# Kernel tuning notes

Hardware: AMD Instinct MI355X
Metric: run time of the kernel (lower is better)

## Reference

```python
import jax, jax.numpy as jnp
import numpy as np

H, D, Kd, Vd = 16, 1024, 64, 64
N, Mlen = 4096, 4096


def setup_inputs() -> dict:
    key = jax.random.key(0)
    ks = jax.random.split(key, 7)
    X = jax.random.normal(ks[0], (N, D), dtype=jnp.float32)
    M = jax.random.normal(ks[1], (Mlen, D), dtype=jnp.float32)
    mask = jax.random.randint(ks[2], (N, Mlen), 0, 2, dtype=jnp.int32)
    Wq = jax.random.normal(ks[3], (H, D, Kd), dtype=jnp.float32)
    Wk = jax.random.normal(ks[4], (H, D, Kd), dtype=jnp.float32)
    Wv = jax.random.normal(ks[5], (H, D, Vd), dtype=jnp.float32)
    Wo = jax.random.normal(ks[6], (H, Vd, D), dtype=jnp.float32)
    return {"X": X, "M": M, "mask": mask, "Wq": Wq, "Wk": Wk, "Wv": Wv, "Wo": Wo}


def reference(X, M, mask, Wq, Wk, Wv, Wo):
    # Projections: [h,n,k], [h,m,k], [h,m,v]
    Q = jnp.einsum('nd,hdk->hnk', X, Wq)
    K = jnp.einsum('md,hdk->hmk', M, Wk)
    V = jnp.einsum('md,hdv->hmv', M, Wv)
    # Masked attention (no scaling, matching the source)
    logits = jnp.einsum('hnk,hmk->hnm', Q, K)
    logits = jnp.where(mask[None, :, :] == 0, -jnp.inf, logits)
    weights = jax.nn.softmax(logits, axis=-1)
    O = jnp.einsum('hnm,hmv->hnv', weights, V)
    Y = jnp.einsum('hnv,hvd->nd', O, Wo)
    return Y
```

## Files before the change

kernel.cpp:

```cpp
#include <hip/hip_runtime.h>

typedef _Float16 half8 __attribute__((ext_vector_type(8)));
typedef _Float16 half4 __attribute__((ext_vector_type(4)));
typedef __fp16 fp16x2 __attribute__((ext_vector_type(2)));
typedef short short8 __attribute__((ext_vector_type(8)));
typedef short short4v __attribute__((ext_vector_type(4)));
typedef float floatx4 __attribute__((ext_vector_type(4)));

#define LOG2E 1.4426950408889634f

#define GLDS16(g, l) __builtin_amdgcn_global_load_lds( \
    (const __attribute__((address_space(1))) unsigned int*)(g), \
    (__attribute__((address_space(3))) unsigned int*)(l), 16, 0, 0)

static __device__ __forceinline__ short f2bf(float f){
  union { float f; unsigned u; } v; v.f = f;
  unsigned r = v.u + 0x7fffu + ((v.u >> 16) & 1u);
  return (short)(r >> 16);
}
static __device__ __forceinline__ float bf2f(short s){
  union { unsigned u; float f; } v; v.u = ((unsigned)(unsigned short)s) << 16;
  return v.f;
}

__global__ __launch_bounds__(256) void kconvA(const float* __restrict__ X,
                                              const float* __restrict__ Mm,
                                              short* __restrict__ XFh, short* __restrict__ XFl,
                                              short* __restrict__ MFh, short* __restrict__ MFl){
  int b = blockIdx.x;
  int t = threadIdx.x, w = t >> 6, l = t & 63, quad = l >> 4;
  int srcsel = b >> 8, ntile = b & 255;
  const float* A = srcsel ? Mm : X;
  short* oh = srcsel ? MFh : XFh;
  short* ol = srcsel ? MFl : XFl;
  int row = ntile*16 + (l & 15);
  #pragma unroll
  for (int i = 0; i < 8; i++){
    int kt = w*8 + i;
    const float* p = A + (size_t)row*1024 + kt*32 + quad*8;
    float4 v0 = *(const float4*)p, v1 = *(const float4*)(p + 4);
    float vv[8] = {v0.x,v0.y,v0.z,v0.w,v1.x,v1.y,v1.z,v1.w};
    short8 hh, ll;
    #pragma unroll
    for (int j = 0; j < 8; j++){
      short hb = f2bf(vv[j]); hh[j] = hb; ll[j] = f2bf(vv[j] - bf2f(hb));
    }
    size_t off = ((size_t)kt*256 + ntile)*512 + l*8;
    *(short8*)&oh[off] = hh;
    *(short8*)&ol[off] = ll;
  }
}

__global__ __launch_bounds__(256) void kconvW2(const float* __restrict__ Wq,
                                               const float* __restrict__ Wk,
                                               const float* __restrict__ Wv,
                                               short* __restrict__ WFh, short* __restrict__ WFl){
  __shared__ float T[128][68];
  int bidx = blockIdx.x, g = blockIdx.y;
  int mat = bidx >> 4, h = bidx & 15;
  const float* W = (mat == 0 ? Wq : (mat == 1 ? Wk : Wv)) + (size_t)h*65536;
  int t = threadIdx.x, w = t >> 6, l = t & 63, quad = (l >> 4) & 3, fl = l & 15;
  #pragma unroll
  for (int p = 0; p < 32; p++){
    int idx = p*256 + t, row = idx >> 6, col = idx & 63;
    T[row][col] = W[(size_t)(g*128 + row)*64 + col];
  }
  __syncthreads();
  for (int ktl = 0; ktl < 4; ktl++){
    short8 hh, ll;
    #pragma unroll
    for (int j = 0; j < 8; j++){
      float v = T[ktl*32 + quad*8 + j][w*16 + fl];
      short hb = f2bf(v); hh[j] = hb; ll[j] = f2bf(v - bf2f(hb));
    }
    size_t frag = ((size_t)bidx*32 + g*4 + ktl)*4 + w;
    *(short8*)&WFh[frag*512 + l*8] = hh;
    *(short8*)&WFl[frag*512 + l*8] = ll;
  }
}

__global__ __launch_bounds__(256) void kmaskpack(const int* __restrict__ mask,
                                                 unsigned* __restrict__ bits){
  int w = blockIdx.x * 256 + threadIdx.x;
  const int4* p = (const int4*)(mask + (size_t)w * 32);
  unsigned b = 0;
  #pragma unroll
  for (int i = 0; i < 8; i++){
    int4 v = p[i];
    b |= (v.x ? 1u : 0u) << (i*4);
    b |= (v.y ? 1u : 0u) << (i*4 + 1);
    b |= (v.z ? 1u : 0u) << (i*4 + 2);
    b |= (v.w ? 1u : 0u) << (i*4 + 3);
  }
  bits[w] = b;
}

__global__ __launch_bounds__(256) void ktransw(const float* __restrict__ src,
                                               short* __restrict__ dsth,
                                               int R, int C){
  __shared__ float tile[32][33];
  int r0 = blockIdx.y*32, c0 = blockIdx.x*32;
  int t = threadIdx.x, tr = t >> 3, tc = (t & 7)*4;
  const float* s = src + (size_t)(r0 + tr)*C + c0 + tc;
  #pragma unroll
  for (int i = 0; i < 4; i++) tile[tr][tc + i] = s[i];
  __syncthreads();
  short* dh = dsth + (size_t)(c0 + tr)*R + r0 + tc;
  #pragma unroll
  for (int i = 0; i < 4; i++)
    dh[i] = f2bf(tile[tc + i][tr]);
}

__global__ __launch_bounds__(256,3) void kproj3(
    const short* __restrict__ XFh, const short* __restrict__ XFl,
    const short* __restrict__ MFh, const short* __restrict__ MFl,
    const short* __restrict__ WFh, const short* __restrict__ WFl,
    _Float16* __restrict__ QFh, _Float16* __restrict__ QFl,
    _Float16* __restrict__ KFh, _Float16* __restrict__ KFl,
    _Float16* __restrict__ VF)
{
  __shared__ short AhL[4096], AlL[4096], BhL[4096], BlL[2048];
  int cb = blockIdx.y, rb = blockIdx.x;
  const bool fused = (cb >= 16);
  int h = fused ? (cb - 16) : cb;
  const short* Ah = fused ? MFh : XFh;
  const short* Al = fused ? MFl : XFl;
  int t = threadIdx.x, w = t >> 6, l = t & 63, quad = l >> 4, ln = l & 15;
  floatx4 acc[2][8] = {};
  for (int kt = 0; kt < 32; kt++){
    __syncthreads();
    size_t abase = ((size_t)kt*256 + rb*8)*512;
    #pragma unroll
    for (int i = 0; i < 2; i++){
      int cidx = i*256 + t;
      GLDS16(Ah + abase + cidx*8, &AhL[(i*256 + w*64)*8]);
      GLDS16(Al + abase + cidx*8, &AlL[(i*256 + w*64)*8]);
    }
    size_t bb0 = (((size_t)cb*32 + kt)*4)*512;
    GLDS16(WFh + bb0 + t*8, &BhL[(w*64)*8]);
    GLDS16(WFl + bb0 + t*8, &BlL[(w*64)*8]);
    if (fused){
      size_t bb1 = (((size_t)(cb + 16)*32 + kt)*4)*512;
      GLDS16(WFh + bb1 + t*8, &BhL[(256 + w*64)*8]);
    }
    __syncthreads();
    short8 ah[2], al[2];
    #pragma unroll
    for (int mt = 0; mt < 2; mt++){
      ah[mt] = *(short8*)&AhL[(w*2 + mt)*512 + l*8];
      al[mt] = *(short8*)&AlL[(w*2 + mt)*512 + l*8];
    }
    {
      short8 bh[4], bl[4];
      #pragma unroll
      for (int nt = 0; nt < 4; nt++){
        bh[nt] = *(short8*)&BhL[nt*512 + l*8];
        bl[nt] = *(short8*)&BlL[nt*512 + l*8];
      }
      #pragma unroll
      for (int mt = 0; mt < 2; mt++)
        #pragma unroll
        for (int nt = 0; nt < 4; nt++){
          acc[mt][nt] = __builtin_amdgcn_mfma_f32_16x16x32_bf16(ah[mt], bh[nt], acc[mt][nt], 0, 0, 0);
          acc[mt][nt] = __builtin_amdgcn_mfma_f32_16x16x32_bf16(ah[mt], bl[nt], acc[mt][nt], 0, 0, 0);
          acc[mt][nt] = __builtin_amdgcn_mfma_f32_16x16x32_bf16(al[mt], bh[nt], acc[mt][nt], 0, 0, 0);
        }
    }
    if (fused){
      short8 bh[4];
      #pragma unroll
      for (int nt = 0; nt < 4; nt++)
        bh[nt] = *(short8*)&BhL[(4 + nt)*512 + l*8];
      #pragma unroll
      for (int mt = 0; mt < 2; mt++)
        #pragma unroll
        for (int nt = 0; nt < 4; nt++)
          acc[mt][4+nt] = __builtin_amdgcn_mfma_f32_16x16x32_bf16(ah[mt], bh[nt], acc[mt][4+nt], 0, 0, 0);
    }
  }
  int row0 = rb*128;
  if (!fused){
    #pragma unroll
    for (int mt = 0; mt < 2; mt++)
      #pragma unroll
      for (int nt = 0; nt < 4; nt++)
        #pragma unroll
        for (int rg = 0; rg < 4; rg++){
          int n = row0 + w*32 + mt*16 + quad*4 + rg;
          int c = nt*16 + ln;
          float v = acc[mt][nt][rg] * LOG2E;
          _Float16 hi = (_Float16)v;
          _Float16 lo = (_Float16)(v - (float)hi);
          int lane2 = (n & 15) + (((c >> 3) & 3) << 4);
          size_t off = (((size_t)h*256 + (n >> 4))*2 + (c >> 5))*512 + lane2*8 + (c & 7);
          QFh[off] = hi; QFl[off] = lo;
        }
  } else {
    #pragma unroll
    for (int mt = 0; mt < 2; mt++)
      #pragma unroll
      for (int nt = 0; nt < 4; nt++)
        #pragma unroll
        for (int rg = 0; rg < 4; rg++){
          int n = row0 + w*32 + mt*16 + quad*4 + rg;
          int c = nt*16 + ln;
          float v = acc[mt][nt][rg];
          _Float16 hi = (_Float16)v;
          _Float16 lo = (_Float16)(v - (float)hi);
          int lane2 = (n & 15) + (((c >> 3) & 3) << 4);
          size_t off = (((size_t)h*256 + (n >> 4))*2 + (c >> 5))*512 + lane2*8 + (c & 7);
          KFh[off] = hi; KFl[off] = lo;
        }
    #pragma unroll
    for (int mt = 0; mt < 2; mt++)
      #pragma unroll
      for (int ntv = 0; ntv < 4; ntv++){
        union { fp16x2 h2[2]; unsigned u2[2]; } pu;
        pu.h2[0] = __builtin_amdgcn_cvt_pkrtz(acc[mt][4+ntv][0], acc[mt][4+ntv][1]);
        pu.h2[1] = __builtin_amdgcn_cvt_pkrtz(acc[mt][4+ntv][2], acc[mt][4+ntv][3]);
        size_t base = (((size_t)h*32 + rb)*16 + ntv*4 + w)*512;
        *(uint2*)&VF[base + (quad*16 + ln)*8 + mt*4] = *(uint2*)&pu.u2[0];
      }
  }
}

__global__ __launch_bounds__(256,4) void kattn8(
    const _Float16* __restrict__ QFh, const _Float16* __restrict__ QFl,
    const _Float16* __restrict__ KFh, const _Float16* __restrict__ KFl,
    const _Float16* __restrict__ VF, const unsigned* __restrict__ bits,
    short* __restrict__ Ows)
{
  __shared__ _Float16 KBh[2][4096], KBl[2][4096], VB[4096];
  int bx = blockIdx.x, h = bx & 15, qb = bx >> 4, q0 = qb*64;
  int t = threadIdx.x, w = t >> 6, l = t & 63, quad = l >> 4, ln = l & 15;

  half8 qh[2], ql[2];
  #pragma unroll
  for (int kc = 0; kc < 2; kc++){
    size_t off = (((size_t)h*256 + qb*4 + w)*2 + kc)*512 + l*8;
    qh[kc] = *(const half8*)&QFh[off];
    ql[kc] = *(const half8*)&QFl[off];
  }

  floatx4 o[4] = {};
  float mst = -1e30f, lst = 0.f;

  const size_t hb = (size_t)h*262144;
  const int cidx0 = t, cidx1 = 256 + t;
  const int ld0 = (w*64)*8, ld1 = (256 + w*64)*8;

  {
    GLDS16(KFh + hb + cidx0*8, &KBh[0][ld0]);
    GLDS16(KFh + hb + cidx1*8, &KBh[0][ld1]);
    GLDS16(KFl + hb + cidx0*8, &KBl[0][ld0]);
    GLDS16(KFl + hb + cidx1*8, &KBl[0][ld1]);
    #pragma unroll
    for (int i = 0; i < 2; i++){
      int cidx = i*256 + t;
      int lu = cidx >> 6, uoff = (cidx & 63)*8;
      int gu = (lu >> 1)*4 + (lu & 1);
      GLDS16(VF + hb + (size_t)gu*512 + uoff, &VB[(i*256 + w*64)*8]);
    }
  }
  uint2 mwv = *(const uint2*)&bits[(size_t)(q0 + w*16 + ln)*128];
  __syncthreads();

  int cur = 0;
  for (int kt = 0; kt < 64; kt++){
    int ktn = (kt + 1) & 63;
    size_t kbn = hb + (size_t)ktn*4096;
    GLDS16(KFh + kbn + cidx0*8, &KBh[cur^1][ld0]);
    GLDS16(KFh + kbn + cidx1*8, &KBh[cur^1][ld1]);
    GLDS16(KFl + kbn + cidx0*8, &KBl[cur^1][ld0]);
    GLDS16(KFl + kbn + cidx1*8, &KBl[cur^1][ld1]);
    uint2 mwn = *(const uint2*)&bits[(size_t)(q0 + w*16 + ln)*128 + ktn*2];

    floatx4 st[4] = {};
    __builtin_amdgcn_s_setprio(1);
    #pragma unroll
    for (int kc = 0; kc < 2; kc++)
      #pragma unroll
      for (int m8 = 0; m8 < 4; m8++){
        half8 kh = *(half8*)&KBh[cur][(m8*2 + kc)*512 + l*8];
        half8 kl = *(half8*)&KBl[cur][(m8*2 + kc)*512 + l*8];
        st[m8] = __builtin_amdgcn_mfma_f32_16x16x32_f16(kh, qh[kc], st[m8], 0, 0, 0);
        st[m8] = __builtin_amdgcn_mfma_f32_16x16x32_f16(kl, qh[kc], st[m8], 0, 0, 0);
        st[m8] = __builtin_amdgcn_mfma_f32_16x16x32_f16(kh, ql[kc], st[m8], 0, 0, 0);
      }
    __builtin_amdgcn_s_setprio(0);

    {
      const unsigned mwp[2] = {mwv.x, mwv.y};
      #pragma unroll
      for (int m8 = 0; m8 < 4; m8++){
        unsigned nib = (mwp[m8 >> 1] >> ((m8 & 1)*16 + quad*4)) & 15u;
        #pragma unroll
        for (int rg = 0; rg < 4; rg++)
          if (!((nib >> rg) & 1u)) st[m8][rg] = -1e30f;
      }
      float a0 = fmaxf(fmaxf(st[0][0], st[0][1]), fmaxf(st[0][2], st[0][3]));
      float a1 = fmaxf(fmaxf(st[1][0], st[1][1]), fmaxf(st[1][2], st[1][3]));
      float a2 = fmaxf(fmaxf(st[2][0], st[2][1]), fmaxf(st[2][2], st[2][3]));
      float a3 = fmaxf(fmaxf(st[3][0], st[3][1]), fmaxf(st[3][2], st[3][3]));
      float mx = fmaxf(fmaxf(a0, a1), fmaxf(a2, a3));
      mx = fmaxf(mx, __shfl_xor(mx, 16));
      mx = fmaxf(mx, __shfl_xor(mx, 32));
      if (__any(mx > mst + 8.0f)){
        float mnew = fmaxf(mst, mx);
        float alpha = exp2f(mst - mnew);
        mst = mnew;
        lst *= alpha;
        #pragma unroll
        for (int vt = 0; vt < 4; vt++) o[vt] *= alpha;
      }
      float ssum = 0.f;
      #pragma unroll
      for (int m8 = 0; m8 < 4; m8++)
        #pragma unroll
        for (int rg = 0; rg < 4; rg++){
          float p = exp2f(st[m8][rg] - mst);
          st[m8][rg] = p; ssum += p;
        }
      lst += ssum;
    }
    mwv = mwn;

    __syncthreads();

    __builtin_amdgcn_s_setprio(1);
    #pragma unroll
    for (int p = 0; p < 2; p++){
      half8 vfp[4];
      #pragma unroll
      for (int vt = 0; vt < 4; vt++)
        vfp[vt] = *(half8*)&VB[((vt*2 + p)*512) + l*8];
      #pragma unroll
      for (int sub = 0; sub < 2; sub++){
        int m8 = p*2 + sub;
        union { fp16x2 h2[2]; half4 h4; } pu;
        pu.h2[0] = __builtin_amdgcn_cvt_pkrtz(st[m8][0], st[m8][1]);
        pu.h2[1] = __builtin_amdgcn_cvt_pkrtz(st[m8][2], st[m8][3]);
        #pragma unroll
        for (int vt = 0; vt < 4; vt++){
          half4 va = sub ? __builtin_shufflevector(vfp[vt], vfp[vt], 4,5,6,7)
                         : __builtin_shufflevector(vfp[vt], vfp[vt], 0,1,2,3);
          o[vt] = __builtin_amdgcn_mfma_f32_16x16x16f16(va, pu.h4, o[vt], 0, 0, 0);
        }
      }
    }
    __builtin_amdgcn_s_setprio(0);

    __syncthreads();

    {
      size_t vbn = hb + (size_t)(ktn >> 1)*8192;
      int vhalf = (ktn & 1)*2;
      #pragma unroll
      for (int i = 0; i < 2; i++){
        int cidx = i*256 + t;
        int lu = cidx >> 6, uoff = (cidx & 63)*8;
        int gu = (lu >> 1)*4 + vhalf + (lu & 1);
        GLDS16(VF + vbn + (size_t)gu*512 + uoff, &VB[(i*256 + w*64)*8]);
      }
    }
    cur ^= 1;
  }

  {
    lst += __shfl_xor(lst, 16);
    lst += __shfl_xor(lst, 32);
    float inv = (lst > 0.f) ? (1.f / lst) : 0.f;
    int n = q0 + w*16 + ln;
    #pragma unroll
    for (int vt = 0; vt < 4; vt++){
      short4v pk;
      #pragma unroll
      for (int rg = 0; rg < 4; rg++) pk[rg] = f2bf(o[vt][rg]*inv);
      *(short4v*)&Ows[(size_t)n*1024 + h*64 + vt*16 + quad*4] = pk;
    }
  }
}

__global__ __launch_bounds__(256,2) void kfinal(const short* __restrict__ Ain,
                                                const short* __restrict__ Bt,
                                                float* __restrict__ Y)
{
  __shared__ short Al[128*48];
  __shared__ short Bl[64*48];
  int cb = blockIdx.y, rb = blockIdx.x;
  int row0 = rb*128, col0 = cb*64;
  int t = threadIdx.x, w = t >> 6, l = t & 63, quad = l >> 4, ln = l & 15;
  floatx4 acc[2][4] = {};
  for (int d0 = 0; d0 < 1024; d0 += 32){
    #pragma unroll
    for (int i = 0; i < 2; i++){
      int u = t + i*256, r = u >> 2, s = u & 3;
      *(int4*)&Al[r*48 + s*8] = *(const int4*)&Ain[(size_t)(row0 + r)*1024 + d0 + s*8];
    }
    { int r = t >> 2, s = t & 3;
      *(int4*)&Bl[r*48 + s*8] = *(const int4*)&Bt[(size_t)(col0 + r)*1024 + d0 + s*8]; }
    __syncthreads();
    short8 bf[4];
    #pragma unroll
    for (int nt = 0; nt < 4; nt++) bf[nt] = *(short8*)&Bl[(nt*16 + ln)*48 + quad*8];
    #pragma unroll
    for (int mt = 0; mt < 2; mt++){
      short8 af = *(short8*)&Al[(w*32 + mt*16 + ln)*48 + quad*8];
      #pragma unroll
      for (int nt = 0; nt < 4; nt++)
        acc[mt][nt] = __builtin_amdgcn_mfma_f32_16x16x32_bf16(af, bf[nt], acc[mt][nt], 0, 0, 0);
    }
    __syncthreads();
  }
  #pragma unroll
  for (int mt = 0; mt < 2; mt++)
    #pragma unroll
    for (int nt = 0; nt < 4; nt++)
      #pragma unroll
      for (int rg = 0; rg < 4; rg++){
        int n = row0 + w*32 + mt*16 + quad*4 + rg;
        int c = col0 + nt*16 + ln;
        Y[(size_t)n*1024 + c] = acc[mt][nt][rg];
      }
}

extern "C" void kernel_launch(void* const* d_in, const int* in_sizes, int n_in,
                              void* d_out, int out_size, void* d_ws, size_t ws_size,
                              hipStream_t stream){
  (void)in_sizes; (void)n_in; (void)out_size; (void)ws_size;
  const float* X    = (const float*)d_in[0];
  const float* Mm   = (const float*)d_in[1];
  const int*   mask = (const int*)d_in[2];
  const float* Wq   = (const float*)d_in[3];
  const float* Wk   = (const float*)d_in[4];
  const float* Wv   = (const float*)d_in[5];
  const float* Wo   = (const float*)d_in[6];
  float* Y = (float*)d_out;
  char* ws = (char*)d_ws;
  const size_t MB = 1024*1024;
  short*    XFh   = (short*)   (ws +  0*MB);
  short*    XFl   = (short*)   (ws +  8*MB);
  short*    MFh   = (short*)   (ws + 16*MB);
  short*    MFl   = (short*)   (ws + 24*MB);
  short*    WFh   = (short*)   (ws + 32*MB);
  short*    WFl   = (short*)   (ws + 38*MB);
  unsigned* bits  = (unsigned*)(ws + 44*MB);
  _Float16* QFh   = (_Float16*)(ws + 46*MB);
  _Float16* QFl   = (_Float16*)(ws + 54*MB);
  _Float16* KFh   = (_Float16*)(ws + 62*MB);
  _Float16* KFl   = (_Float16*)(ws + 70*MB);
  _Float16* VF    = (_Float16*)(ws + 78*MB);
  short*    Ows   = (short*)   (ws +  0*MB);
  short*    Wot   = (short*)   (ws +  8*MB);

  kconvA<<<512, 256, 0, stream>>>(X, Mm, XFh, XFl, MFh, MFl);
  kconvW2<<<dim3(48,8), 256, 0, stream>>>(Wq, Wk, Wv, WFh, WFl);
  kmaskpack<<<2048, 256, 0, stream>>>(mask, bits);
  kproj3<<<dim3(32,32), 256, 0, stream>>>(XFh, XFl, MFh, MFl, WFh, WFl,
                                          QFh, QFl, KFh, KFl, VF);
  ktransw<<<dim3(32,32), 256, 0, stream>>>(Wo, Wot, 1024, 1024);
  kattn8<<<1024, 256, 0, stream>>>(QFh, QFl, KFh, KFl, VF, bits, Ows);
  kfinal<<<dim3(32,16), 256, 0, stream>>>(Ows, Wot, Y);
}
```

Before: 458.4 us.

## Split key tile across wave pairs, each wave handling two query tiles

Restructures the attention kernel so each wave processes two 16-row query tiles against half of each 64-key tile, rather than one query tile against the full key tile. Each K fragment loaded from LDS is reused across two query tiles, and each V fragment load is halved. The two waves' partial softmax states and outputs are merged at the end through LDS. The cost is more registers (Q, O and the running max and sum are doubled) and an extra LDS-based combine step with a sync.

```diff
diff --git a/kernel.cpp b/kernel.cpp
--- a/kernel.cpp
+++ b/kernel.cpp
@@ -224,7 +224,7 @@
   }
 }
 
-__global__ __launch_bounds__(256,4) void kattn8(
+__global__ __launch_bounds__(256,4) void kattn10(
     const _Float16* __restrict__ QFh, const _Float16* __restrict__ QFl,
     const _Float16* __restrict__ KFh, const _Float16* __restrict__ KFl,
     const _Float16* __restrict__ VF, const unsigned* __restrict__ bits,
@@ -233,17 +233,20 @@
   __shared__ _Float16 KBh[2][4096], KBl[2][4096], VB[4096];
   int bx = blockIdx.x, h = bx & 15, qb = bx >> 4, q0 = qb*64;
   int t = threadIdx.x, w = t >> 6, l = t & 63, quad = l >> 4, ln = l & 15;
-
-  half8 qh[2], ql[2];
-  #pragma unroll
-  for (int kc = 0; kc < 2; kc++){
-    size_t off = (((size_t)h*256 + qb*4 + w)*2 + kc)*512 + l*8;
-    qh[kc] = *(const half8*)&QFh[off];
-    ql[kc] = *(const half8*)&QFl[off];
-  }
-
-  floatx4 o[4] = {};
-  float mst = -1e30f, lst = 0.f;
+  int qpair = w >> 1, khalf = w & 1;
+
+  half8 qh[2][2], ql[2][2];
+  #pragma unroll
+  for (int nt2 = 0; nt2 < 2; nt2++)
+    #pragma unroll
+    for (int kc = 0; kc < 2; kc++){
+      size_t off = (((size_t)h*256 + qb*4 + qpair*2 + nt2)*2 + kc)*512 + l*8;
+      qh[nt2][kc] = *(const half8*)&QFh[off];
+      ql[nt2][kc] = *(const half8*)&QFl[off];
+    }
+
+  floatx4 o[2][4] = {};
+  float mst[2] = {-1e30f, -1e30f}, lst[2] = {0.f, 0.f};
 
   const size_t hb = (size_t)h*262144;
   const int cidx0 = t, cidx1 = 256 + t;
@@ -262,7 +265,9 @@
       GLDS16(VF + hb + (size_t)gu*512 + uoff, &VB[(i*256 + w*64)*8]);
     }
   }
-  uint2 mwv = *(const uint2*)&bits[(size_t)(q0 + w*16 + ln)*128];
+  unsigned mwv[2];
+  mwv[0] = bits[(size_t)(q0 + qpair*32 + ln)*128 + khalf];
+  mwv[1] = bits[(size_t)(q0 + qpair*32 + 16 + ln)*128 + khalf];
   __syncthreads();
 
   int cur = 0;
@@ -273,80 +278,83 @@
     GLDS16(KFh + kbn + cidx1*8, &KBh[cur^1][ld1]);
     GLDS16(KFl + kbn + cidx0*8, &KBl[cur^1][ld0]);
     GLDS16(KFl + kbn + cidx1*8, &KBl[cur^1][ld1]);
-    uint2 mwn = *(const uint2*)&bits[(size_t)(q0 + w*16 + ln)*128 + ktn*2];
-
-    floatx4 st[4] = {};
+    unsigned mwn0 = bits[(size_t)(q0 + qpair*32 + ln)*128 + ktn*2 + khalf];
+    unsigned mwn1 = bits[(size_t)(q0 + qpair*32 + 16 + ln)*128 + ktn*2 + khalf];
+
+    floatx4 st[2][2] = {};
     __builtin_amdgcn_s_setprio(1);
     #pragma unroll
     for (int kc = 0; kc < 2; kc++)
       #pragma unroll
-      for (int m8 = 0; m8 < 4; m8++){
-        half8 kh = *(half8*)&KBh[cur][(m8*2 + kc)*512 + l*8];
-        half8 kl = *(half8*)&KBl[cur][(m8*2 + kc)*512 + l*8];
-        st[m8] = __builtin_amdgcn_mfma_f32_16x16x32_f16(kh, qh[kc], st[m8], 0, 0, 0);
-        st[m8] = __builtin_amdgcn_mfma_f32_16x16x32_f16(kl, qh[kc], st[m8], 0, 0, 0);
-        st[m8] = __builtin_amdgcn_mfma_f32_16x16x32_f16(kh, ql[kc], st[m8], 0, 0, 0);
+      for (int mm = 0; mm < 2; mm++){
+        int r = ((khalf*2 + mm)*2 + kc)*512 + l*8;
+        half8 kh = *(half8*)&KBh[cur][r];
+        half8 kl = *(half8*)&KBl[cur][r];
+        #pragma unroll
+        for (int nt2 = 0; nt2 < 2; nt2++){
+          st[nt2][mm] = __builtin_amdgcn_mfma_f32_16x16x32_f16(kh, qh[nt2][kc], st[nt2][mm], 0, 0, 0);
+          st[nt2][mm] = __builtin_amdgcn_mfma_f32_16x16x32_f16(kl, qh[nt2][kc], st[nt2][mm], 0, 0, 0);
+          st[nt2][mm] = __builtin_amdgcn_mfma_f32_16x16x32_f16(kh, ql[nt2][kc], st[nt2][mm], 0, 0, 0);
+        }
       }
     __builtin_amdgcn_s_setprio(0);
 
-    {
-      const unsigned mwp[2] = {mwv.x, mwv.y};
-      #pragma unroll
-      for (int m8 = 0; m8 < 4; m8++){
-        unsigned nib = (mwp[m8 >> 1] >> ((m8 & 1)*16 + quad*4)) & 15u;
+    #pragma unroll
+    for (int nt2 = 0; nt2 < 2; nt2++){
+      #pragma unroll
+      for (int mm = 0; mm < 2; mm++){
+        unsigned nib = (mwv[nt2] >> (mm*16 + quad*4)) & 15u;
         #pragma unroll
         for (int rg = 0; rg < 4; rg++)
-          if (!((nib >> rg) & 1u)) st[m8][rg] = -1e30f;
-      }
-      float a0 = fmaxf(fmaxf(st[0][0], st[0][1]), fmaxf(st[0][2], st[0][3]));
-      float a1 = fmaxf(fmaxf(st[1][0], st[1][1]), fmaxf(st[1][2], st[1][3]));
-      float a2 = fmaxf(fmaxf(st[2][0], st[2][1]), fmaxf(st[2][2], st[2][3]));
-      float a3 = fmaxf(fmaxf(st[3][0], st[3][1]), fmaxf(st[3][2], st[3][3]));
-      float mx = fmaxf(fmaxf(a0, a1), fmaxf(a2, a3));
+          if (!((nib >> rg) & 1u)) st[nt2][mm][rg] = -1e30f;
+      }
+      float a0 = fmaxf(fmaxf(st[nt2][0][0], st[nt2][0][1]), fmaxf(st[nt2][0][2], st[nt2][0][3]));
+      float a1 = fmaxf(fmaxf(st[nt2][1][0], st[nt2][1][1]), fmaxf(st[nt2][1][2], st[nt2][1][3]));
+      float mx = fmaxf(a0, a1);
       mx = fmaxf(mx, __shfl_xor(mx, 16));
       mx = fmaxf(mx, __shfl_xor(mx, 32));
-      if (__any(mx > mst + 8.0f)){
-        float mnew = fmaxf(mst, mx);
-        float alpha = exp2f(mst - mnew);
-        mst = mnew;
-        lst *= alpha;
-        #pragma unroll
-        for (int vt = 0; vt < 4; vt++) o[vt] *= alpha;
+      if (__any(mx > mst[nt2] + 8.0f)){
+        float mnew = fmaxf(mst[nt2], mx);
+        float alpha = exp2f(mst[nt2] - mnew);
+        mst[nt2] = mnew;
+        lst[nt2] *= alpha;
+        #pragma unroll
+        for (int vt = 0; vt < 4; vt++) o[nt2][vt] *= alpha;
       }
       float ssum = 0.f;
       #pragma unroll
-      for (int m8 = 0; m8 < 4; m8++)
+      for (int mm = 0; mm < 2; mm++)
         #pragma unroll
         for (int rg = 0; rg < 4; rg++){
-          float p = exp2f(st[m8][rg] - mst);
-          st[m8][rg] = p; ssum += p;
-        }
-      lst += ssum;
-    }
-    mwv = mwn;
+          float p = exp2f(st[nt2][mm][rg] - mst[nt2]);
+          st[nt2][mm][rg] = p; ssum += p;
+        }
+      lst[nt2] += ssum;
+    }
+    mwv[0] = mwn0; mwv[1] = mwn1;
 
     __syncthreads();
 
     __builtin_amdgcn_s_setprio(1);
-    #pragma unroll
-    for (int p = 0; p < 2; p++){
+    {
       half8 vfp[4];
       #pragma unroll
       for (int vt = 0; vt < 4; vt++)
-        vfp[vt] = *(half8*)&VB[((vt*2 + p)*512) + l*8];
-      #pragma unroll
-      for (int sub = 0; sub < 2; sub++){
-        int m8 = p*2 + sub;
-        union { fp16x2 h2[2]; half4 h4; } pu;
-        pu.h2[0] = __builtin_amdgcn_cvt_pkrtz(st[m8][0], st[m8][1]);
-        pu.h2[1] = __builtin_amdgcn_cvt_pkrtz(st[m8][2], st[m8][3]);
-        #pragma unroll
-        for (int vt = 0; vt < 4; vt++){
-          half4 va = sub ? __builtin_shufflevector(vfp[vt], vfp[vt], 4,5,6,7)
-                         : __builtin_shufflevector(vfp[vt], vfp[vt], 0,1,2,3);
-          o[vt] = __builtin_amdgcn_mfma_f32_16x16x16f16(va, pu.h4, o[vt], 0, 0, 0);
-        }
-      }
+        vfp[vt] = *(half8*)&VB[((vt*2 + khalf)*512) + l*8];
+      #pragma unroll
+      for (int mm = 0; mm < 2; mm++)
+        #pragma unroll
+        for (int nt2 = 0; nt2 < 2; nt2++){
+          union { fp16x2 h2[2]; half4 h4; } pu;
+          pu.h2[0] = __builtin_amdgcn_cvt_pkrtz(st[nt2][mm][0], st[nt2][mm][1]);
+          pu.h2[1] = __builtin_amdgcn_cvt_pkrtz(st[nt2][mm][2], st[nt2][mm][3]);
+          #pragma unroll
+          for (int vt = 0; vt < 4; vt++){
+            half4 va = mm ? __builtin_shufflevector(vfp[vt], vfp[vt], 4,5,6,7)
+                          : __builtin_shufflevector(vfp[vt], vfp[vt], 0,1,2,3);
+            o[nt2][vt] = __builtin_amdgcn_mfma_f32_16x16x16f16(va, pu.h4, o[nt2][vt], 0, 0, 0);
+          }
+        }
     }
     __builtin_amdgcn_s_setprio(0);
 
@@ -366,16 +374,39 @@
     cur ^= 1;
   }
 
+  __syncthreads();
   {
-    lst += __shfl_xor(lst, 16);
-    lst += __shfl_xor(lst, 32);
-    float inv = (lst > 0.f) ? (1.f / lst) : 0.f;
-    int n = q0 + w*16 + ln;
+    float* cbo = (w < 2) ? (float*)&KBh[0][0] : (float*)&KBl[0][0];
+    int wi = w & 1, wpi = wi ^ 1;
+    #pragma unroll
+    for (int nt2 = 0; nt2 < 2; nt2++)
+      #pragma unroll
+      for (int vt = 0; vt < 4; vt++)
+        *(floatx4*)&cbo[wi*2048 + (nt2*4 + vt)*256 + l*4] = o[nt2][vt];
+    float* cbm = (float*)&VB[0];
+    cbm[w*256 + l*4 + 0] = mst[0];
+    cbm[w*256 + l*4 + 1] = lst[0];
+    cbm[w*256 + l*4 + 2] = mst[1];
+    cbm[w*256 + l*4 + 3] = lst[1];
+    __syncthreads();
+    int wp = w ^ 1;
+    int myn = khalf;
+    float pm = cbm[wp*256 + l*4 + myn*2 + 0];
+    float pl = cbm[wp*256 + l*4 + myn*2 + 1];
+    float m  = fmaxf(mst[myn], pm);
+    float as = exp2f(mst[myn] - m), ap = exp2f(pm - m);
+    float lc = lst[myn]*as + pl*ap;
+    lc += __shfl_xor(lc, 16);
+    lc += __shfl_xor(lc, 32);
+    float inv = (lc > 0.f) ? (1.f / lc) : 0.f;
+    int n = q0 + qpair*32 + myn*16 + ln;
     #pragma unroll
     for (int vt = 0; vt < 4; vt++){
+      floatx4 po = *(floatx4*)&cbo[wpi*2048 + (myn*4 + vt)*256 + l*4];
       short4v pk;
       #pragma unroll
-      for (int rg = 0; rg < 4; rg++) pk[rg] = f2bf(o[vt][rg]*inv);
+      for (int rg = 0; rg < 4; rg++)
+        pk[rg] = f2bf((o[myn][vt][rg]*as + po[rg]*ap) * inv);
       *(short4v*)&Ows[(size_t)n*1024 + h*64 + vt*16 + quad*4] = pk;
     }
   }
@@ -459,6 +490,6 @@
   kproj3<<<dim3(32,32), 256, 0, stream>>>(XFh, XFl, MFh, MFl, WFh, WFl,
                                           QFh, QFl, KFh, KFl, VF);
   ktransw<<<dim3(32,32), 256, 0, stream>>>(Wo, Wot, 1024, 1024);
-  kattn8<<<1024, 256, 0, stream>>>(QFh, QFl, KFh, KFl, VF, bits, Ows);
+  kattn10<<<1024, 256, 0, stream>>>(QFh, QFl, KFh, KFl, VF, bits, Ows);
   kfinal<<<dim3(32,16), 256, 0, stream>>>(Ows, Wot, Y);
 }
```

Measured after the change: 589.1 us. +28.5%, slower.
